# Optimization experiments

Measured on AMD Instinct MI355X. Metric: run time of the kernel, lower is better.

Reference implementation:

```python
import jax, jax.numpy as jnp
import numpy as np

N_HEADS = 16


def setup_inputs() -> dict:
    key = jax.random.key(0)
    k1, k2, k3 = jax.random.split(key, 3)
    B, N, D = 2, 2048, 1024
    x = jax.random.normal(k1, (B, N, D), dtype=jnp.float32)
    w_qkv = jax.random.normal(k2, (D, 3 * D), dtype=jnp.float32) * (D ** -0.5)
    w_proj = jax.random.normal(k3, (D, D), dtype=jnp.float32) * (D ** -0.5)
    return {"x": x, "w_qkv": w_qkv, "w_proj": w_proj}


def _rotate_half(t):
    # interleaved-pair rotation: (x1, x2) -> (-x2, x1)
    shp = t.shape
    t2 = t.reshape(*shp[:-1], shp[-1] // 2, 2)
    return jnp.stack((-t2[..., 1], t2[..., 0]), axis=-1).reshape(shp)


def reference(x, w_qkv, w_proj):
    B, N, D = x.shape
    H = N_HEADS
    hd = D // H
    qkv = x @ w_qkv                                   # [B, N, 3D]
    qkv = qkv.reshape(B, N, 3, H, hd).transpose(2, 0, 3, 1, 4)
    q, k, v = qkv[0], qkv[1], qkv[2]                  # [B, H, N, hd]

    inv_freq = 1.0 / (10000.0 ** (jnp.arange(0, hd, 2, dtype=jnp.float32) / hd))
    freqs = jnp.arange(N, dtype=jnp.float32)[:, None] * inv_freq[None, :]  # [N, hd/2]
    sin = jnp.repeat(jnp.sin(freqs), 2, axis=-1)[None, None]               # [1,1,N,hd]
    cos = jnp.repeat(jnp.cos(freqs), 2, axis=-1)[None, None]

    q = q * cos + _rotate_half(q) * sin
    k = k * cos + _rotate_half(k) * sin

    scale = hd ** -0.5
    attn = jax.nn.softmax(jnp.einsum('bhqd,bhkd->bhqk', q, k) * scale, axis=-1)
    out = jnp.einsum('bhqk,bhkd->bhqd', attn, v)      # [B, H, N, hd]
    out = out.transpose(0, 2, 1, 3).reshape(B, N, D)
    return out @ w_proj
```

## Files before the change

kernel.cpp:

```cpp
#include <hip/hip_runtime.h>
#include <hip/hip_bf16.h>
#include <cstdint>
#include <cmath>

#define DEVINL __device__ __forceinline__

typedef __attribute__((ext_vector_type(8)))  __bf16 b8;
typedef __attribute__((ext_vector_type(4)))  float  f4;
typedef __attribute__((ext_vector_type(16))) float  f16v;
typedef __attribute__((ext_vector_type(4)))  unsigned int u32x4;

DEVINL unsigned short f2bf(float f){
  unsigned int u = __float_as_uint(f);
  u += 0x7FFFu + ((u >> 16) & 1u);
  return (unsigned short)(u >> 16);
}

DEVINL void gl_lds16(const void* g, void* l){
  __builtin_amdgcn_global_load_lds(
      (const __attribute__((address_space(1))) void*)g,
      (__attribute__((address_space(3))) void*)l, 16, 0, 0);
}

DEVINL f4 mfma16(b8 a, b8 b, f4 c){
  return __builtin_amdgcn_mfma_f32_16x16x32_bf16(a, b, c, 0, 0, 0);
}
DEVINL f16v mfma32(b8 a, b8 b, f16v c){
  return __builtin_amdgcn_mfma_f32_32x32x16_bf16(a, b, c, 0, 0, 0);
}

DEVINL float exp2a(float x){
  float r; asm("v_exp_f32 %0, %1" : "=v"(r) : "v"(x)); return r;
}
DEVINL unsigned int cvtpk(float lo, float hi){
  unsigned int r; asm("v_cvt_pk_bf16_f32 %0, %1, %2" : "=v"(r) : "v"(lo), "v"(hi)); return r;
}
DEVINL void plswap(unsigned int &a, unsigned int &b){
  asm("v_permlane32_swap_b32 %0, %1" : "+v"(a), "+v"(b));
}

#define BARRAW() asm volatile("s_barrier" ::: "memory")
#define WCNT(N)  asm volatile("s_waitcnt vmcnt(" #N ")" ::: "memory")


__global__ __launch_bounds__(256) void cast_bf16_k(const float* __restrict__ in,
                                                   unsigned short* __restrict__ out, int n4){
  int stride = gridDim.x * blockDim.x;
  for (int i = blockIdx.x * blockDim.x + threadIdx.x; i < n4; i += stride){
    float4 v = ((const float4*)in)[i];
    ushort4 o; o.x = f2bf(v.x); o.y = f2bf(v.y); o.z = f2bf(v.z); o.w = f2bf(v.w);
    ((ushort4*)out)[i] = o;
  }
}

__global__ __launch_bounds__(256) void transpose_cast_k(const float* __restrict__ in,
                                                        unsigned short* __restrict__ out,
                                                        int K, int N){
  __shared__ float t[32][33];
  int nx = blockIdx.x * 32, kx = blockIdx.y * 32;
  int tx = threadIdx.x & 31, ty = threadIdx.x >> 5;
  #pragma unroll
  for (int i = 0; i < 4; i++)
    t[ty + 8*i][tx] = in[(size_t)(kx + ty + 8*i) * N + nx + tx];
  __syncthreads();
  #pragma unroll
  for (int i = 0; i < 4; i++)
    out[(size_t)(nx + ty + 8*i) * K + kx + tx] = f2bf(t[tx][ty + 8*i]);
}

__global__ __launch_bounds__(256) void rope_tab_k(float2* __restrict__ rt){
  int t = blockIdx.x * 256 + threadIdx.x;
  int n = t >> 5, i = t & 31;
  float invf = expf(-(float)i * (9.210340371976184f / 32.0f));
  float ph = (float)n * invf;
  float s, c;
  sincosf(ph, &s, &c);
  rt[t] = make_float2(c, s);
}


template<int NREP, int EPI>
__global__ __launch_bounds__(512, 2) void gemm256_k(const unsigned short* __restrict__ A,
                                                    const unsigned short* __restrict__ Bt, int N,
                                                    float* __restrict__ Of,
                                                    unsigned short* __restrict__ Qg,
                                                    unsigned short* __restrict__ Kg,
                                                    unsigned short* __restrict__ Vt,
                                                    const float2* __restrict__ rtab){
  constexpr int K = 1024;
  __shared__ unsigned short As[2][256 * 64];
  __shared__ unsigned short Bs[2][NREP * 64 * 64];
  const int tid = threadIdx.x, w = tid >> 6, l = tid & 63;
  const int wm = w >> 2, wn = w & 3;
  const int id = blockIdx.x + blockIdx.y * 16;
  const int xcd = id & 7, jj2 = id >> 3;
  const int mblk = (xcd >> 1) * 4 + (jj2 >> 3);
  const int nblk = (xcd & 1) * 8 + (jj2 & 7);
  const int m0 = mblk * 256, n0 = nblk * (NREP * 64);

  f4 acc[8][NREP];
  const f4 fz = {0.f, 0.f, 0.f, 0.f};
  #pragma unroll
  for (int i = 0; i < 8; i++)
    #pragma unroll
    for (int j = 0; j < NREP; j++) acc[i][j] = fz;

  const int srow8 = (l >> 3);
  const int ssrc  = ((l & 7) ^ (srow8 & 7)) * 8;

  auto stage = [&](int slot, int kt){
    const unsigned short* Ab = A + kt * 64 + ssrc;
    #pragma unroll
    for (int c2 = 0; c2 < 4; c2++){
      int ch = w * 4 + c2;
      gl_lds16(Ab + (size_t)(m0 + ch * 8 + srow8) * K, (char*)&As[slot][0] + ch * 1024);
    }
    const unsigned short* Bb = Bt + kt * 64 + ssrc;
    #pragma unroll
    for (int c2 = 0; c2 < NREP; c2++){
      int ch = w * NREP + c2;
      gl_lds16(Bb + (size_t)(n0 + ch * 8 + srow8) * K, (char*)&Bs[slot][0] + ch * 1024);
    }
  };

  auto compute = [&](int slot){
    const char* At  = (const char*)&As[slot][0];
    const char* Btl = (const char*)&Bs[slot][0];
    #pragma unroll
    for (int kk = 0; kk < 2; kk++){
      b8 af[8], bf[NREP];
      int sb = kk * 4 + (l >> 4);
      #pragma unroll
      for (int mi = 0; mi < 8; mi++){
        int r = wm * 128 + mi * 16 + (l & 15);
        af[mi] = *(const b8*)(At + r * 128 + ((sb ^ (r & 7)) * 16));
      }
      #pragma unroll
      for (int ni = 0; ni < NREP; ni++){
        int r = wn * (NREP * 16) + ni * 16 + (l & 15);
        bf[ni] = *(const b8*)(Btl + r * 128 + ((sb ^ (r & 7)) * 16));
      }
      __builtin_amdgcn_s_setprio(1);
      #pragma unroll
      for (int mi = 0; mi < 8; mi++)
        #pragma unroll
        for (int ni = 0; ni < NREP; ni++)
          acc[mi][ni] = mfma16(af[mi], bf[ni], acc[mi][ni]);
      __builtin_amdgcn_s_setprio(0);
    }
  };

  auto wcnt_stg = [&](){
    if constexpr (NREP == 4)      WCNT(8);
    else if constexpr (NREP == 3) WCNT(7);
    else if constexpr (NREP == 2) WCNT(6);
    else                          WCNT(5);
  };

  stage(0, 0);
  stage(1, 1);
  wcnt_stg();
  BARRAW();
  for (int i = 0; i < 8; i++){
    compute(0);
    BARRAW();
    if (i < 7){ stage(0, 2 * i + 2); wcnt_stg(); }
    else      { WCNT(0); }
    BARRAW();
    compute(1);
    BARRAW();
    if (i < 7){ stage(1, 2 * i + 3); wcnt_stg(); }
    BARRAW();
  }

  if constexpr (EPI == 0){
    const float qscale = 0.18033688011112042f;
    const int bb2 = m0 >> 11;
    #pragma unroll
    for (int mi = 0; mi < 8; mi++){
      #pragma unroll
      for (int ni = 0; ni < NREP; ni++){
        f4 a = acc[mi][ni];
        int c = n0 + wn * (NREP * 16) + ni * 16 + (l & 15);
        int s = c >> 10;
        int d = c & 63, h = (c >> 6) & 15;
        if (s == 2){
          int ns0 = (m0 & 2047) + wm * 128 + mi * 16 + (l >> 4) * 4;
          ushort4 pv;
          pv.x = f2bf(a[0]); pv.y = f2bf(a[1]); pv.z = f2bf(a[2]); pv.w = f2bf(a[3]);
          *(ushort4*)(Vt + (((size_t)(bb2 * 16 + h) * 64 + d) << 11) + ns0) = pv;
        } else {
          #pragma unroll
          for (int jj = 0; jj < 4; jj++){
            int m = m0 + wm * 128 + mi * 16 + (l >> 4) * 4 + jj;
            int bb = m >> 11, ns = m & 2047;
            size_t didx = ((size_t)(bb * 16 + h) * 2048 + ns) * 64 + d;
            float part = __shfl_xor(a[jj], 1);
            float2 cs = rtab[ns * 32 + (d >> 1)];
            float val = (d & 1) ? (a[jj] * cs.x + part * cs.y)
                                : (a[jj] * cs.x - part * cs.y);
            if (s == 0){ Qg[didx] = f2bf(val * qscale); }
            else       { Kg[didx] = f2bf(val); }
          }
        }
      }
    }
  } else {
    #pragma unroll
    for (int mi = 0; mi < 8; mi++)
      #pragma unroll
      for (int ni = 0; ni < NREP; ni++){
        int c = n0 + wn * (NREP * 16) + ni * 16 + (l & 15);
        #pragma unroll
        for (int jj = 0; jj < 4; jj++){
          int m = m0 + wm * 128 + mi * 16 + (l >> 4) * 4 + jj;
          Of[(size_t)m * N + c] = acc[mi][ni][jj];
        }
      }
  }
}


__global__ __launch_bounds__(256) void attn_k(const unsigned short* __restrict__ Qg,
                                              const unsigned short* __restrict__ Kg,
                                              const unsigned short* __restrict__ Vt,
                                              unsigned short* __restrict__ Ao){
  __shared__ unsigned short Ks[2][4096];
  __shared__ unsigned short Vs[2][4096];
  const int tid = threadIdx.x, w = tid >> 6, l = tid & 63;
  const int l31 = l & 31, lam = l >> 5;

  const int id = blockIdx.x + blockIdx.y * 16;
  const int xc = id & 7, j = id >> 3;
  const int g = xc * 4 + (j & 3), qb = j >> 2;
  const int q0 = qb * 128 + w * 32;
  const size_t hb = (size_t)g << 17;

  b8 qf[4];
  {
    const unsigned short* qrow = Qg + hb + (size_t)(q0 + l31) * 64 + lam * 8;
    #pragma unroll
    for (int kd = 0; kd < 4; kd++) qf[kd] = *(const b8*)(qrow + kd * 16);
  }

  const unsigned short* kgb = Kg + hb;
  const unsigned short* vgb = Vt + hb;
  const int srow = (l >> 3);
  const int sc8  = ((l & 7) ^ (srow & 7)) * 8;

  auto stage = [&](int buf, int kv0){
    #pragma unroll
    for (int c = 0; c < 2; c++){
      int chunk = w * 2 + c;
      int r = chunk * 8 + srow;
      gl_lds16(kgb + (size_t)(kv0 + r) * 64 + sc8,
               (char*)&Ks[buf][0] + chunk * 1024);
      gl_lds16(vgb + (size_t)r * 2048 + kv0 + sc8,
               (char*)&Vs[buf][0] + chunk * 1024);
    }
  };

  union { u32x4 u; b8 v; } ones;
  ones.u[0] = ones.u[1] = ones.u[2] = ones.u[3] = 0x3F803F80u;

  f16v O[2], L;
  #pragma unroll
  for (int i = 0; i < 16; i++){ O[0][i] = 0.f; O[1][i] = 0.f; L[i] = 0.f; }

  auto tile = [&](int buf){
    b8 kf[8], vf[8];
    const char* ksb = (const char*)&Ks[buf][0];
    const char* vsb = (const char*)&Vs[buf][0];
    const int rsw = (l31 & 7);
    #pragma unroll
    for (int kvb = 0; kvb < 2; kvb++)
      #pragma unroll
      for (int kd = 0; kd < 4; kd++)
        kf[kvb * 4 + kd] = *(const b8*)(ksb + (kvb * 32 + l31) * 128
                                        + (((kd * 2 + lam) ^ rsw) * 16));
    #pragma unroll
    for (int s = 0; s < 4; s++)
      #pragma unroll
      for (int db = 0; db < 2; db++)
        vf[s * 2 + db] = *(const b8*)(vsb + (db * 32 + l31) * 128
                                      + (((2 * s + lam) ^ rsw) * 16));

    f16v st[2];
    #pragma unroll
    for (int i = 0; i < 16; i++){ st[0][i] = 0.f; st[1][i] = 0.f; }
    #pragma unroll
    for (int kd = 0; kd < 4; kd++) st[0] = mfma32(kf[kd],     qf[kd], st[0]);
    #pragma unroll
    for (int kd = 0; kd < 4; kd++) st[1] = mfma32(kf[4 + kd], qf[kd], st[1]);

    #pragma unroll
    for (int b2 = 0; b2 < 2; b2++)
      #pragma unroll
      for (int r = 0; r < 16; r++)
        st[b2][r] = exp2a(st[b2][r]);

    #pragma unroll
    for (int s = 0; s < 4; s++){
      const int b = s >> 1, base = (s & 1) * 8;
      unsigned int pA = cvtpk(st[b][base + 0], st[b][base + 1]);
      unsigned int pB = cvtpk(st[b][base + 2], st[b][base + 3]);
      unsigned int pC = cvtpk(st[b][base + 4], st[b][base + 5]);
      unsigned int pD = cvtpk(st[b][base + 6], st[b][base + 7]);
      plswap(pA, pC); plswap(pB, pD);
      union { u32x4 u; b8 v; } pf;
      pf.u[0] = pA; pf.u[1] = pB; pf.u[2] = pC; pf.u[3] = pD;
      O[0] = mfma32(pf.v, vf[s * 2 + 0], O[0]);
      O[1] = mfma32(pf.v, vf[s * 2 + 1], O[1]);
      L    = mfma32(pf.v, ones.v,       L);
    }
  };

  stage(0, 0);
  stage(1, 64);
  WCNT(4);
  BARRAW();
  for (int i = 0; i < 16; i++){
    tile(0);
    BARRAW();
    if (i < 15){ stage(0, (2 * i + 2) * 64); WCNT(4); }
    else       { WCNT(0); }
    BARRAW();
    tile(1);
    BARRAW();
    if (i < 15){ stage(1, (2 * i + 3) * 64); WCNT(4); }
    BARRAW();
  }

  const int bb = g >> 4, h = g & 15;
  unsigned short* aoBase = Ao + (size_t)bb * 2048 * 1024 + h * 64 + l31;
  #pragma unroll
  for (int r = 0; r < 16; r++){
    int qr = (r & 3) + 8 * (r >> 2) + 4 * lam;
    float li = 1.0f / L[r];
    size_t rowoff = (size_t)(q0 + qr) * 1024;
    aoBase[rowoff]      = f2bf(O[0][r] * li);
    aoBase[rowoff + 32] = f2bf(O[1][r] * li);
  }
}


extern "C" void kernel_launch(void* const* d_in, const int* in_sizes, int n_in,
                              void* d_out, int out_size, void* d_ws, size_t ws_size,
                              hipStream_t stream){
  const float* x     = (const float*)d_in[0];
  const float* wqkv  = (const float*)d_in[1];
  const float* wproj = (const float*)d_in[2];
  float* out = (float*)d_out;

  if (ws_size < 42467328u) return;
  char* ws = (char*)d_ws;
  unsigned short* xb     = (unsigned short*)(ws);
  unsigned short* wqkvT  = (unsigned short*)(ws + 8388608);
  unsigned short* wprojT = (unsigned short*)(ws + 14680064);
  float2*         rtab   = (float2*)(ws + 16777216);
  unsigned short* Qg     = (unsigned short*)(ws + 17301504);
  unsigned short* Kg     = (unsigned short*)(ws + 25690112);
  unsigned short* Vt     = (unsigned short*)(ws + 34078720);
  unsigned short* Ao     = xb;

  cast_bf16_k<<<2048, 256, 0, stream>>>(x, xb, 4096 * 1024 / 4);
  transpose_cast_k<<<dim3(96, 32), 256, 0, stream>>>(wqkv, wqkvT, 1024, 3072);
  transpose_cast_k<<<dim3(32, 32), 256, 0, stream>>>(wproj, wprojT, 1024, 1024);
  rope_tab_k<<<256, 256, 0, stream>>>(rtab);
  gemm256_k<3, 0><<<dim3(16, 16), 512, 0, stream>>>(xb, wqkvT, 3072, nullptr, Qg, Kg, Vt, rtab);
  attn_k<<<dim3(16, 32), 256, 0, stream>>>(Qg, Kg, Vt, Ao);
  gemm256_k<1, 1><<<dim3(16, 16), 512, 0, stream>>>(Ao, wprojT, 1024, out, nullptr, nullptr, nullptr, nullptr);
}
```

Before: 115.2 us.

## Triple-buffer attention K/V staging and merge prep kernels into one launch

The attention loop moves from double to triple buffering of K/V tiles in shared memory, issuing the next load before computing the current tile and using a single barrier per tile instead of two. The four preprocessing kernels (x cast, two weight transpose-casts, rope table) are merged into one launch that splits work by block index. This targets barrier stalls and launch overhead, at the cost of more LDS per attention block, which may limit occupancy.

```diff
diff --git a/kernel.cpp b/kernel.cpp
--- a/kernel.cpp
+++ b/kernel.cpp
@@ -43,39 +43,47 @@
 #define WCNT(N)  asm volatile("s_waitcnt vmcnt(" #N ")" ::: "memory")
 
 
-__global__ __launch_bounds__(256) void cast_bf16_k(const float* __restrict__ in,
-                                                   unsigned short* __restrict__ out, int n4){
-  int stride = gridDim.x * blockDim.x;
-  for (int i = blockIdx.x * blockDim.x + threadIdx.x; i < n4; i += stride){
-    float4 v = ((const float4*)in)[i];
-    ushort4 o; o.x = f2bf(v.x); o.y = f2bf(v.y); o.z = f2bf(v.z); o.w = f2bf(v.w);
-    ((ushort4*)out)[i] = o;
-  }
-}
-
-__global__ __launch_bounds__(256) void transpose_cast_k(const float* __restrict__ in,
-                                                        unsigned short* __restrict__ out,
-                                                        int K, int N){
+__global__ __launch_bounds__(256) void prep_k(const float* __restrict__ x,
+                                              const float* __restrict__ wqkv,
+                                              const float* __restrict__ wproj,
+                                              unsigned short* __restrict__ xb,
+                                              unsigned short* __restrict__ wqkvT,
+                                              unsigned short* __restrict__ wprojT,
+                                              float2* __restrict__ rtab){
   __shared__ float t[32][33];
-  int nx = blockIdx.x * 32, kx = blockIdx.y * 32;
-  int tx = threadIdx.x & 31, ty = threadIdx.x >> 5;
-  #pragma unroll
-  for (int i = 0; i < 4; i++)
-    t[ty + 8*i][tx] = in[(size_t)(kx + ty + 8*i) * N + nx + tx];
-  __syncthreads();
-  #pragma unroll
-  for (int i = 0; i < 4; i++)
-    out[(size_t)(nx + ty + 8*i) * K + kx + tx] = f2bf(t[tx][ty + 8*i]);
-}
-
-__global__ __launch_bounds__(256) void rope_tab_k(float2* __restrict__ rt){
-  int t = blockIdx.x * 256 + threadIdx.x;
-  int n = t >> 5, i = t & 31;
-  float invf = expf(-(float)i * (9.210340371976184f / 32.0f));
-  float ph = (float)n * invf;
-  float s, c;
-  sincosf(ph, &s, &c);
-  rt[t] = make_float2(c, s);
+  const int b = blockIdx.x, tid = threadIdx.x;
+  if (b < 1024){
+    int i = b * 256 + tid;
+    #pragma unroll
+    for (int it = 0; it < 4; it++){
+      float4 v = ((const float4*)x)[i];
+      ushort4 o; o.x = f2bf(v.x); o.y = f2bf(v.y); o.z = f2bf(v.z); o.w = f2bf(v.w);
+      ((ushort4*)xb)[i] = o;
+      i += 1024 * 256;
+    }
+  } else if (b < 5120){
+    const float* in; unsigned short* out; int N2, tt;
+    if (b < 4096){ in = wqkv;  out = wqkvT;  N2 = 3072; tt = b - 1024; }
+    else         { in = wproj; out = wprojT; N2 = 1024; tt = b - 4096; }
+    const int K2 = 1024;
+    int nx = (tt % (N2 / 32)) * 32, kx = (tt / (N2 / 32)) * 32;
+    int tx = tid & 31, ty = tid >> 5;
+    #pragma unroll
+    for (int i2 = 0; i2 < 4; i2++)
+      t[ty + 8 * i2][tx] = in[(size_t)(kx + ty + 8 * i2) * N2 + nx + tx];
+    __syncthreads();
+    #pragma unroll
+    for (int i2 = 0; i2 < 4; i2++)
+      out[(size_t)(nx + ty + 8 * i2) * K2 + kx + tx] = f2bf(t[tx][ty + 8 * i2]);
+  } else {
+    int tr = (b - 5120) * 256 + tid;
+    int n = tr >> 5, i2 = tr & 31;
+    float invf = expf(-(float)i2 * (9.210340371976184f / 32.0f));
+    float ph = (float)n * invf;
+    float s, c;
+    sincosf(ph, &s, &c);
+    rtab[tr] = make_float2(c, s);
+  }
 }
 
 
@@ -225,8 +233,8 @@
                                               const unsigned short* __restrict__ Kg,
                                               const unsigned short* __restrict__ Vt,
                                               unsigned short* __restrict__ Ao){
-  __shared__ unsigned short Ks[2][4096];
-  __shared__ unsigned short Vs[2][4096];
+  __shared__ unsigned short Ks[3][4096];
+  __shared__ unsigned short Vs[3][4096];
   const int tid = threadIdx.x, w = tid >> 6, l = tid & 63;
   const int l31 = l & 31, lam = l >> 5;
 
@@ -315,21 +323,17 @@
     }
   };
 
-  stage(0, 0);
-  stage(1, 64);
-  WCNT(4);
-  BARRAW();
-  for (int i = 0; i < 16; i++){
-    tile(0);
-    BARRAW();
-    if (i < 15){ stage(0, (2 * i + 2) * 64); WCNT(4); }
-    else       { WCNT(0); }
-    BARRAW();
-    tile(1);
-    BARRAW();
-    if (i < 15){ stage(1, (2 * i + 3) * 64); WCNT(4); }
-    BARRAW();
-  }
+  stage(0, 0); stage(1, 64);
+  WCNT(4); BARRAW();
+  #pragma unroll 1
+  for (int t = 0; t < 30; t += 3){
+    stage(2, (t + 2) * 64); tile(0); WCNT(4); BARRAW();
+    stage(0, (t + 3) * 64); tile(1); WCNT(4); BARRAW();
+    stage(1, (t + 4) * 64); tile(2); WCNT(4); BARRAW();
+  }
+  tile(0);
+  WCNT(0); BARRAW();
+  tile(1);
 
   const int bb = g >> 4, h = g & 15;
   unsigned short* aoBase = Ao + (size_t)bb * 2048 * 1024 + h * 64 + l31;
@@ -363,10 +367,7 @@
   unsigned short* Vt     = (unsigned short*)(ws + 34078720);
   unsigned short* Ao     = xb;
 
-  cast_bf16_k<<<2048, 256, 0, stream>>>(x, xb, 4096 * 1024 / 4);
-  transpose_cast_k<<<dim3(96, 32), 256, 0, stream>>>(wqkv, wqkvT, 1024, 3072);
-  transpose_cast_k<<<dim3(32, 32), 256, 0, stream>>>(wproj, wprojT, 1024, 1024);
-  rope_tab_k<<<256, 256, 0, stream>>>(rtab);
+  prep_k<<<5376, 256, 0, stream>>>(x, wqkv, wproj, xb, wqkvT, wprojT, rtab);
   gemm256_k<3, 0><<<dim3(16, 16), 512, 0, stream>>>(xb, wqkvT, 3072, nullptr, Qg, Kg, Vt, rtab);
   attn_k<<<dim3(16, 32), 256, 0, stream>>>(Qg, Kg, Vt, Ao);
   gemm256_k<1, 1><<<dim3(16, 16), 512, 0, stream>>>(Ao, wprojT, 1024, out, nullptr, nullptr, nullptr, nullptr);
```

Result: faster. 111.3 us (-3.4%).
